# Kernel optimization log

Measured on AMD Instinct MI355X. Metric: run time of the kernel, lower is better.

The kernel has to match this reference:

```python
import jax, jax.numpy as jnp
import numpy as np

N_NODES = 50000
N_EDGES = 800000
IN_F = 128
OUT_F = 32
HEADS = 4
NEG_SLOPE = 0.2


def setup_inputs() -> dict:
    key = jax.random.key(0)
    ks = jax.random.split(key, 6)
    x = jax.random.normal(ks[0], (N_NODES, IN_F), dtype=jnp.float32)
    edge_index = jax.random.randint(ks[1], (2, N_EDGES), 0, N_NODES, dtype=jnp.int64)
    s = 1.0 / np.sqrt(IN_F)
    W_l = jax.random.normal(ks[2], (IN_F, HEADS * OUT_F), dtype=jnp.float32) * s
    W_r = jax.random.normal(ks[3], (IN_F, HEADS * OUT_F), dtype=jnp.float32) * s
    att = jax.random.normal(ks[4], (HEADS, OUT_F), dtype=jnp.float32) * s
    bias = jax.random.normal(ks[5], (HEADS * OUT_F,), dtype=jnp.float32) * 0.01
    return {"x": x, "edge_index": edge_index, "W_l": W_l, "W_r": W_r, "att": att, "bias": bias}


def reference(x, edge_index, W_l, W_r, att, bias):
    N = x.shape[0]
    # add self loops (PyG GATv2Conv default add_self_loops=True)
    loops = jnp.arange(N, dtype=edge_index.dtype)
    src = jnp.concatenate([edge_index[0], loops])
    dst = jnp.concatenate([edge_index[1], loops])
    # node projections: [N, H, C]
    xl = (x @ W_l).reshape(N, HEADS, OUT_F)
    xr = (x @ W_r).reshape(N, HEADS, OUT_F)
    # edge-wise GATv2 attention logits
    e = jax.nn.leaky_relu(xl[src] + xr[dst], NEG_SLOPE)  # [E, H, C]
    logits = jnp.einsum('ehc,hc->eh', e, att)  # [E, H]
    # segment softmax over destination nodes
    m = jax.ops.segment_max(logits, dst, num_segments=N)  # [N, H]
    ex = jnp.exp(logits - m[dst])
    denom = jax.ops.segment_sum(ex, dst, num_segments=N)  # [N, H]
    alpha = ex / (denom[dst] + 1e-16)  # [E, H]
    # weighted scatter-aggregate of source messages
    msg = xl[src] * alpha[:, :, None]  # [E, H, C]
    out = jax.ops.segment_sum(msg, dst, num_segments=N)  # [N, H, C]
    return out.reshape(N, HEADS * OUT_F) + bias
```

## Files before the change

### kernel.cpp

```cpp
#include <hip/hip_runtime.h>
#include <math.h>

#define IN_F 128
#define OUT_F 32
#define HEADS 4
#define HC 128
#define NEG_SLOPE 0.2f
#define LOG2E 1.44269504088896f
#define ALD 136
#define HB 256
#define BINS_U32 16384
#define NPP 65536

typedef short bf16x8 __attribute__((ext_vector_type(8)));
typedef float f32x4 __attribute__((ext_vector_type(4)));

__device__ __forceinline__ unsigned short f2bf(float f) {
    unsigned u = __float_as_uint(f);
    u += 0x7FFFu + ((u >> 16) & 1u);
    return (unsigned short)(u >> 16);
}

__global__ void __launch_bounds__(256)
prep_kernel(const float* __restrict__ Wl, const float* __restrict__ Wr,
            unsigned short* __restrict__ Wt, unsigned int* __restrict__ cursor) {
    const int t0 = blockIdx.x * 256 + threadIdx.x;
    const int stride = gridDim.x * 256;
    for (int i = t0; i < 256 * IN_F; i += stride) {
        const int n = i >> 7, k = i & 127;
        const float v = (n < 128) ? Wl[k * 128 + n] : Wr[k * 128 + (n - 128)];
        Wt[i] = f2bf(v);
    }
    if (t0 == 0) *cursor = 0u;
}

__global__ void __launch_bounds__(256)
proj_kernel(const float* __restrict__ x,
            const unsigned short* __restrict__ Wt,
            unsigned short* __restrict__ xlb,
            float* __restrict__ xr, int N) {
    __shared__ unsigned short As[64 * ALD];
    const int tid = threadIdx.x;
    const int n0 = blockIdx.x * 64;
#pragma unroll
    for (int q = 0; q < 8; ++q) {
        const int idx = q * 256 + tid;
        const int row = idx >> 5;
        const int col4 = (idx & 31) * 4;
        const float4 v = *(const float4*)&x[(size_t)min(n0 + row, N - 1) * IN_F + col4];
        ushort4 p;
        p.x = f2bf(v.x); p.y = f2bf(v.y); p.z = f2bf(v.z); p.w = f2bf(v.w);
        *(ushort4*)&As[row * ALD + col4] = p;
    }
    __syncthreads();

    const int w = tid >> 6, lane = tid & 63;
    const int lm = lane & 15, lg = lane >> 4;

    bf16x8 af[4];
#pragma unroll
    for (int kk = 0; kk < 4; ++kk)
        af[kk] = *(const bf16x8*)&As[(w * 16 + lm) * ALD + kk * 32 + lg * 8];

    f32x4 acc[16];
#pragma unroll
    for (int c = 0; c < 16; ++c) acc[c] = (f32x4){0.f, 0.f, 0.f, 0.f};

#pragma unroll
    for (int c = 0; c < 16; ++c) {
#pragma unroll
        for (int kk = 0; kk < 4; ++kk) {
            const bf16x8 bf = *(const bf16x8*)&Wt[(size_t)(c * 16 + lm) * 128 + kk * 32 + lg * 8];
            acc[c] = __builtin_amdgcn_mfma_f32_16x16x32_bf16(af[kk], bf, acc[c], 0, 0, 0);
        }
    }

    const int rbase = n0 + w * 16 + lg * 4;
#pragma unroll
    for (int c = 0; c < 16; ++c) {
#pragma unroll
        for (int r = 0; r < 4; ++r) {
            const int R = rbase + r;
            if (R >= N) continue;
            const int C = c * 16 + lm;
            if (c < 8) xlb[(size_t)R * HC + C] = f2bf(acc[c][r]);
            else       xr[(size_t)R * HC + (C - 128)] = acc[c][r];
        }
    }
}

__global__ void __launch_bounds__(512)
hist_kernel(const int* __restrict__ ei, unsigned char* __restrict__ hist,
            int N, int E0, int Etot) {
    __shared__ unsigned int h[BINS_U32];
    const int b = blockIdx.x;
    const int epb = (Etot + HB - 1) / HB;
    const int t0 = b * epb, t1 = min(t0 + epb, Etot);
    for (int i = threadIdx.x; i < BINS_U32; i += 512) h[i] = 0u;
    __syncthreads();
    for (int t = t0 + threadIdx.x; t < t1; t += 512) {
        const int dst = (t < E0) ? ei[E0 + t] : (t - E0);
        atomicAdd(&h[dst >> 2], 1u << ((dst & 3) * 8));
    }
    __syncthreads();
    unsigned int* row = (unsigned int*)&hist[(size_t)b * N];
    const int nw = N >> 2;
    for (int i = threadIdx.x; i < nw; i += 512) row[i] = h[i];
}

__global__ void __launch_bounds__(256)
reduce_alloc_kernel(unsigned char* __restrict__ hist, int* __restrict__ deg,
                    int* __restrict__ start, unsigned int* __restrict__ cursor,
                    int N) {
    __shared__ int sc[256];
    __shared__ int base_s;
    const int tid = threadIdx.x;
    const int n = blockIdx.x * 256 + tid;
    int run = 0;
    if (n < N) {
#pragma unroll 8
        for (int b = 0; b < HB; ++b) {
            const size_t idx = (size_t)b * N + n;
            const int t = hist[idx];
            hist[idx] = (unsigned char)run;
            run += t;
        }
        deg[n] = run;
    }
    sc[tid] = run;
    __syncthreads();
#pragma unroll
    for (int off = 1; off < 256; off <<= 1) {
        int v = (tid >= off) ? sc[tid - off] : 0;
        __syncthreads();
        sc[tid] += v;
        __syncthreads();
    }
    if (tid == 255) base_s = (int)atomicAdd(cursor, (unsigned int)sc[255]);
    __syncthreads();
    if (n < N) start[n] = base_s + sc[tid] - run;
}

__global__ void __launch_bounds__(512)
scatter2_kernel(const int* __restrict__ ei, const int* __restrict__ start,
                const unsigned char* __restrict__ hist, int* __restrict__ esrc,
                int N, int E0, int Etot) {
    __shared__ unsigned int f[BINS_U32];
    const int b = blockIdx.x;
    const int epb = (Etot + HB - 1) / HB;
    const int t0 = b * epb, t1 = min(t0 + epb, Etot);
    for (int i = threadIdx.x; i < BINS_U32; i += 512) f[i] = 0u;
    __syncthreads();
    for (int t = t0 + threadIdx.x; t < t1; t += 512) {
        int src, dst;
        if (t < E0) { src = ei[t]; dst = ei[E0 + t]; }
        else        { src = dst = t - E0; }
        const unsigned sh = (dst & 3) * 8;
        const unsigned old = atomicAdd(&f[dst >> 2], 1u << sh);
        const unsigned local = (old >> sh) & 0xFFu;
        const int pos = start[dst] + (int)hist[(size_t)b * N + dst] + (int)local;
        esrc[pos] = src;
    }
}

template <int CTRL>
__device__ __forceinline__ float dpp_add(float v) {
    const int t = __builtin_amdgcn_update_dpp(
        0, __float_as_int(v), CTRL, 0xF, 0xF, true);
    return v + __int_as_float(t);
}

__device__ __forceinline__ float row_sum_bcast(float c) {
    c = dpp_add<0xB1>(c);
    c = dpp_add<0x4E>(c);
    c = dpp_add<0x124>(c);
    c = dpp_add<0x128>(c);
    return c;
}

__global__ void __launch_bounds__(256)
fused_agg_kernel(const unsigned short* __restrict__ xlb,
                 const float* __restrict__ xr,
                 const float* __restrict__ att,
                 const float* __restrict__ bias,
                 const int* __restrict__ esrc,
                 const int* __restrict__ start,
                 const int* __restrict__ deg,
                 float* __restrict__ out, int N, int EtotM1) {
    const int wid = threadIdx.x >> 6;
    const int lane = threadIdx.x & 63;
    const int n = blockIdx.x * 4 + wid;
    if (n >= N) return;

    const int ch = lane * 2;
    const float2 xr2 = *(const float2*)&xr[(size_t)n * HC + ch];
    const float2 at2 = *(const float2*)&att[ch];
    const float au0 = at2.x * LOG2E, au1 = at2.y * LOG2E;
    const int s0 = start[n];
    const int d = deg[n];

    float sum = 0.f, ax = 0.f, ay = 0.f;

    auto body = [&](unsigned pk) {
        const float vx = __uint_as_float(pk << 16);
        const float vy = __uint_as_float(pk & 0xFFFF0000u);
        const float sx = vx + xr2.x;
        const float sy = vy + xr2.y;
        const float lx = fmaxf(sx, sx * NEG_SLOPE);
        const float ly = fmaxf(sy, sy * NEG_SLOPE);
        const float c = fmaf(au1, ly, au0 * lx);
        const float p = __builtin_amdgcn_exp2f(row_sum_bcast(c));
        sum += p;
        ax = fmaf(p, vx, ax);
        ay = fmaf(p, vy, ay);
    };

    for (int jb = 0; jb < d; jb += 64) {
        const int cnt = min(64, d - jb);
        const int ev = esrc[min(s0 + jb + lane, EtotM1)];

        unsigned pk0 = *(const unsigned*)&xlb[(size_t)__builtin_amdgcn_readlane(ev, 0) * HC + ch];
        unsigned pk1 = *(const unsigned*)&xlb[(size_t)__builtin_amdgcn_readlane(ev, 1) * HC + ch];
        unsigned pk2 = *(const unsigned*)&xlb[(size_t)__builtin_amdgcn_readlane(ev, 2) * HC + ch];
        unsigned pk3 = *(const unsigned*)&xlb[(size_t)__builtin_amdgcn_readlane(ev, 3) * HC + ch];

        int j = 0;
        for (; j + 3 < cnt; j += 4) {
            const unsigned q0 = *(const unsigned*)&xlb[(size_t)__builtin_amdgcn_readlane(ev, min(j + 4, 63)) * HC + ch];
            const unsigned q1 = *(const unsigned*)&xlb[(size_t)__builtin_amdgcn_readlane(ev, min(j + 5, 63)) * HC + ch];
            const unsigned q2 = *(const unsigned*)&xlb[(size_t)__builtin_amdgcn_readlane(ev, min(j + 6, 63)) * HC + ch];
            const unsigned q3 = *(const unsigned*)&xlb[(size_t)__builtin_amdgcn_readlane(ev, min(j + 7, 63)) * HC + ch];
            body(pk0); body(pk1); body(pk2); body(pk3);
            pk0 = q0; pk1 = q1; pk2 = q2; pk3 = q3;
        }
        for (; j < cnt; ++j) {
            body(pk0);
            pk0 = pk1; pk1 = pk2; pk2 = pk3;
        }
    }
    const float inv = __builtin_amdgcn_rcpf(sum + 1e-16f);
    const float2 b2 = *(const float2*)&bias[ch];
    float2 o;
    o.x = fmaf(ax, inv, b2.x);
    o.y = fmaf(ay, inv, b2.y);
    *(float2*)&out[(size_t)n * HC + ch] = o;
}

extern "C" void kernel_launch(void* const* d_in, const int* in_sizes, int n_in,
                              void* d_out, int out_size, void* d_ws, size_t ws_size,
                              hipStream_t stream) {
    const float* x    = (const float*)d_in[0];
    const int*   ei   = (const int*)d_in[1];
    const float* Wl   = (const float*)d_in[2];
    const float* Wr   = (const float*)d_in[3];
    const float* att  = (const float*)d_in[4];
    const float* bias = (const float*)d_in[5];
    float* out        = (float*)d_out;

    const int N    = in_sizes[0] / IN_F;
    const int E0   = in_sizes[1] / 2;
    const int Etot = E0 + N;

    char* base = (char*)d_ws;
    unsigned short* xlb = (unsigned short*)base; base += (size_t)N * HC * sizeof(unsigned short);
    float* xr   = (float*)base;        base += (size_t)N * HC * sizeof(float);
    int*   esrc = (int*)base;          base += (size_t)Etot * sizeof(int);
    int*   strt = (int*)base;          base += (size_t)N * sizeof(int);
    int*   deg  = (int*)base;          base += (size_t)N * sizeof(int);
    unsigned char* hist = (unsigned char*)base; base += (size_t)HB * N * sizeof(unsigned char);
    unsigned short* Wt = (unsigned short*)base; base += 256 * IN_F * sizeof(unsigned short);
    unsigned int* cursor = (unsigned int*)base;

    prep_kernel<<<128, 256, 0, stream>>>(Wl, Wr, Wt, cursor);
    proj_kernel<<<(N + 63) / 64, 256, 0, stream>>>(x, Wt, xlb, xr, N);
    hist_kernel<<<HB, 512, 0, stream>>>(ei, hist, N, E0, Etot);
    reduce_alloc_kernel<<<(N + 255) / 256, 256, 0, stream>>>(hist, deg, strt, cursor, N);
    scatter2_kernel<<<HB, 512, 0, stream>>>(ei, strt, hist, esrc, N, E0, Etot);

    fused_agg_kernel<<<(N + 3) / 4, 256, 0, stream>>>(xlb, xr, att, bias, esrc, strt, deg,
                                                      out, N, Etot - 1);
}
```

Measured before the change: 223.9 us.

## Fuse weight prep into histogram, record per-edge ranks, vectorize prefix reduce

Weight transposition and cursor reset move into the histogram kernel, which removes one launch. The histogram pass now stores each edge's local rank in a byte array, so the scatter kernel no longer redoes the shared-memory atomics and the LDS clear. The reduce/alloc kernel handles four nodes per thread with packed 32-bit reads and int4 writes. In exchange there is an extra Etot-byte rank buffer, an extra write and read of it, and the code now assumes N is divisible by 4.

```diff
diff --git a/kernel.cpp b/kernel.cpp
--- a/kernel.cpp
+++ b/kernel.cpp
@@ -10,7 +10,6 @@
 #define ALD 136
 #define HB 256
 #define BINS_U32 16384
-#define NPP 65536
 
 typedef short bf16x8 __attribute__((ext_vector_type(8)));
 typedef float f32x4 __attribute__((ext_vector_type(4)));
@@ -21,17 +20,36 @@
     return (unsigned short)(u >> 16);
 }
 
-__global__ void __launch_bounds__(256)
-prep_kernel(const float* __restrict__ Wl, const float* __restrict__ Wr,
-            unsigned short* __restrict__ Wt, unsigned int* __restrict__ cursor) {
-    const int t0 = blockIdx.x * 256 + threadIdx.x;
-    const int stride = gridDim.x * 256;
-    for (int i = t0; i < 256 * IN_F; i += stride) {
+__global__ void __launch_bounds__(512)
+hist_kernel(const int* __restrict__ ei, unsigned char* __restrict__ hist,
+            unsigned char* __restrict__ rank8,
+            const float* __restrict__ Wl, const float* __restrict__ Wr,
+            unsigned short* __restrict__ Wt, unsigned int* __restrict__ cursor,
+            int N, int E0, int Etot) {
+    __shared__ unsigned int h[BINS_U32];
+    const int b = blockIdx.x;
+    const int gt = b * 512 + threadIdx.x;
+    for (int i = gt; i < 256 * IN_F; i += HB * 512) {
         const int n = i >> 7, k = i & 127;
         const float v = (n < 128) ? Wl[k * 128 + n] : Wr[k * 128 + (n - 128)];
         Wt[i] = f2bf(v);
     }
-    if (t0 == 0) *cursor = 0u;
+    if (gt == 0) *cursor = 0u;
+
+    const int epb = (Etot + HB - 1) / HB;
+    const int t0 = b * epb, t1 = min(t0 + epb, Etot);
+    for (int i = threadIdx.x; i < BINS_U32; i += 512) h[i] = 0u;
+    __syncthreads();
+    for (int t = t0 + threadIdx.x; t < t1; t += 512) {
+        const int dst = (t < E0) ? ei[E0 + t] : (t - E0);
+        const unsigned sh = (dst & 3) * 8;
+        const unsigned old = atomicAdd(&h[dst >> 2], 1u << sh);
+        rank8[t] = (unsigned char)((old >> sh) & 0xFFu);
+    }
+    __syncthreads();
+    unsigned int* row = (unsigned int*)&hist[(size_t)b * N];
+    const int nw = N >> 2;
+    for (int i = threadIdx.x; i < nw; i += 512) row[i] = h[i];
 }
 
 __global__ void __launch_bounds__(256)
@@ -89,77 +107,61 @@
     }
 }
 
-__global__ void __launch_bounds__(512)
-hist_kernel(const int* __restrict__ ei, unsigned char* __restrict__ hist,
-            int N, int E0, int Etot) {
-    __shared__ unsigned int h[BINS_U32];
-    const int b = blockIdx.x;
-    const int epb = (Etot + HB - 1) / HB;
-    const int t0 = b * epb, t1 = min(t0 + epb, Etot);
-    for (int i = threadIdx.x; i < BINS_U32; i += 512) h[i] = 0u;
-    __syncthreads();
-    for (int t = t0 + threadIdx.x; t < t1; t += 512) {
-        const int dst = (t < E0) ? ei[E0 + t] : (t - E0);
-        atomicAdd(&h[dst >> 2], 1u << ((dst & 3) * 8));
-    }
-    __syncthreads();
-    unsigned int* row = (unsigned int*)&hist[(size_t)b * N];
-    const int nw = N >> 2;
-    for (int i = threadIdx.x; i < nw; i += 512) row[i] = h[i];
-}
-
-__global__ void __launch_bounds__(256)
-reduce_alloc_kernel(unsigned char* __restrict__ hist, int* __restrict__ deg,
+__global__ void __launch_bounds__(64)
+reduce_alloc_kernel(unsigned int* __restrict__ hist32, int* __restrict__ deg,
                     int* __restrict__ start, unsigned int* __restrict__ cursor,
-                    int N) {
-    __shared__ int sc[256];
+                    int N4) {
+    __shared__ int sc[64];
     __shared__ int base_s;
     const int tid = threadIdx.x;
-    const int n = blockIdx.x * 256 + tid;
-    int run = 0;
-    if (n < N) {
+    const int n4 = blockIdx.x * 64 + tid;
+    int r0 = 0, r1 = 0, r2 = 0, r3 = 0;
+    if (n4 < N4) {
 #pragma unroll 8
         for (int b = 0; b < HB; ++b) {
-            const size_t idx = (size_t)b * N + n;
-            const int t = hist[idx];
-            hist[idx] = (unsigned char)run;
-            run += t;
-        }
-        deg[n] = run;
-    }
-    sc[tid] = run;
-    __syncthreads();
-#pragma unroll
-    for (int off = 1; off < 256; off <<= 1) {
+            const size_t idx = (size_t)b * N4 + n4;
+            const unsigned w = hist32[idx];
+            hist32[idx] = (unsigned)(r0 | (r1 << 8) | (r2 << 16) | (r3 << 24));
+            r0 += w & 0xFFu; r1 += (w >> 8) & 0xFFu;
+            r2 += (w >> 16) & 0xFFu; r3 += (w >> 24) & 0xFFu;
+        }
+    }
+    const int tot = r0 + r1 + r2 + r3;
+    sc[tid] = tot;
+    __syncthreads();
+#pragma unroll
+    for (int off = 1; off < 64; off <<= 1) {
         int v = (tid >= off) ? sc[tid - off] : 0;
         __syncthreads();
         sc[tid] += v;
         __syncthreads();
     }
-    if (tid == 255) base_s = (int)atomicAdd(cursor, (unsigned int)sc[255]);
-    __syncthreads();
-    if (n < N) start[n] = base_s + sc[tid] - run;
+    if (tid == 63) base_s = (int)atomicAdd(cursor, (unsigned int)sc[63]);
+    __syncthreads();
+    if (n4 < N4) {
+        const int s = base_s + sc[tid] - tot;
+        int4 st, dg;
+        st.x = s; st.y = s + r0; st.z = st.y + r1; st.w = st.z + r2;
+        dg.x = r0; dg.y = r1; dg.z = r2; dg.w = r3;
+        *(int4*)&start[n4 * 4] = st;
+        *(int4*)&deg[n4 * 4] = dg;
+    }
 }
 
 __global__ void __launch_bounds__(512)
 scatter2_kernel(const int* __restrict__ ei, const int* __restrict__ start,
-                const unsigned char* __restrict__ hist, int* __restrict__ esrc,
-                int N, int E0, int Etot) {
-    __shared__ unsigned int f[BINS_U32];
+                const unsigned char* __restrict__ hist,
+                const unsigned char* __restrict__ rank8,
+                int* __restrict__ esrc, int N, int E0, int Etot) {
     const int b = blockIdx.x;
     const int epb = (Etot + HB - 1) / HB;
     const int t0 = b * epb, t1 = min(t0 + epb, Etot);
-    for (int i = threadIdx.x; i < BINS_U32; i += 512) f[i] = 0u;
-    __syncthreads();
+    const unsigned char* hrow = &hist[(size_t)b * N];
     for (int t = t0 + threadIdx.x; t < t1; t += 512) {
         int src, dst;
         if (t < E0) { src = ei[t]; dst = ei[E0 + t]; }
         else        { src = dst = t - E0; }
-        const unsigned sh = (dst & 3) * 8;
-        const unsigned old = atomicAdd(&f[dst >> 2], 1u << sh);
-        const unsigned local = (old >> sh) & 0xFFu;
-        const int pos = start[dst] + (int)hist[(size_t)b * N + dst] + (int)local;
-        esrc[pos] = src;
+        esrc[start[dst] + (int)hrow[dst] + (int)rank8[t]] = src;
     }
 }
 
@@ -268,15 +270,17 @@
     int*   strt = (int*)base;          base += (size_t)N * sizeof(int);
     int*   deg  = (int*)base;          base += (size_t)N * sizeof(int);
     unsigned char* hist = (unsigned char*)base; base += (size_t)HB * N * sizeof(unsigned char);
+    unsigned char* rank8 = (unsigned char*)base; base += (size_t)Etot * sizeof(unsigned char);
     unsigned short* Wt = (unsigned short*)base; base += 256 * IN_F * sizeof(unsigned short);
     unsigned int* cursor = (unsigned int*)base;
 
-    prep_kernel<<<128, 256, 0, stream>>>(Wl, Wr, Wt, cursor);
+    hist_kernel<<<HB, 512, 0, stream>>>(ei, hist, rank8, Wl, Wr, Wt, cursor,
+                                        N, E0, Etot);
     proj_kernel<<<(N + 63) / 64, 256, 0, stream>>>(x, Wt, xlb, xr, N);
-    hist_kernel<<<HB, 512, 0, stream>>>(ei, hist, N, E0, Etot);
-    reduce_alloc_kernel<<<(N + 255) / 256, 256, 0, stream>>>(hist, deg, strt, cursor, N);
-    scatter2_kernel<<<HB, 512, 0, stream>>>(ei, strt, hist, esrc, N, E0, Etot);
-
+    reduce_alloc_kernel<<<(N / 4 + 63) / 64, 64, 0, stream>>>(
+        (unsigned int*)hist, deg, strt, cursor, N / 4);
+    scatter2_kernel<<<HB, 512, 0, stream>>>(ei, strt, hist, rank8, esrc,
+                                            N, E0, Etot);
     fused_agg_kernel<<<(N + 3) / 4, 256, 0, stream>>>(xlb, xr, att, bias, esrc, strt, deg,
                                                       out, N, Etot - 1);
 }
```

Result: faster. 219.1 us (-2.2%).
